# Performance work log

Hardware: AMD Instinct MI355X
Metric: run time of the kernel (lower is better)

Reference implementation:

```python
import jax, jax.numpy as jnp
import numpy as np

NTASKS = 10
CAP = 3          # semantic_cap_size / num_capsules
SEQ = 128        # max_seq_length / class_dim
HID = 768
ADAPT = 2048
NEG = -10000.0
NUM_ITERS = 3


def squash(t, axis=-1):
    sq = jnp.sum(t * t, axis=axis, keepdims=True)
    return (sq / (1.0 + sq)) * t / jnp.sqrt(sq)


def setup_inputs() -> dict:
    key = jax.random.key(0)
    ks = jax.random.split(key, 12)
    B = 128
    sc = 0.02
    return {
        "x": jax.random.normal(ks[0], (B, SEQ, HID), jnp.float32),
        "t": 5,
        "s": jnp.ones((1,), jnp.float32),
        "fc1_w": jax.random.normal(ks[1], (ADAPT, HID), jnp.float32) * sc,
        "fc1_b": jnp.zeros((ADAPT,), jnp.float32),
        "fc2_w": jax.random.normal(ks[2], (HID, ADAPT), jnp.float32) * sc,
        "fc2_b": jnp.zeros((HID,), jnp.float32),
        "efc1": jax.random.normal(ks[3], (NTASKS, ADAPT), jnp.float32),
        "efc2": jax.random.normal(ks[4], (NTASKS, HID), jnp.float32),
        "sfc1_w": jax.random.normal(ks[5], (NTASKS, 100, HID), jnp.float32) * sc,
        "sfc1_b": jnp.zeros((NTASKS, 100), jnp.float32),
        "sfc2_w": jax.random.normal(ks[6], (NTASKS, CAP, 100), jnp.float32) * sc,
        "sfc2_b": jnp.zeros((NTASKS, CAP), jnp.float32),
        "route_weights": jax.random.normal(ks[7], (CAP, NTASKS, SEQ * CAP, SEQ), jnp.float32),
        "larger_w": jax.random.normal(ks[8], (HID, CAP), jnp.float32) * sc,
        "larger_b": jnp.zeros((HID,), jnp.float32),
        "elarger": jax.random.normal(ks[9], (NTASKS, HID), jnp.float32),
    }


def reference(x, t, s, fc1_w, fc1_b, fc2_w, fc2_b, efc1, efc2,
              sfc1_w, sfc1_b, sfc2_w, sfc2_b, route_weights,
              larger_w, larger_b, elarger):
    B = x.shape[0]
    # ---- semantic capsules: per-task two-layer linear (no activation) ----
    h1 = jnp.einsum('blh,nkh->nblk', x, sfc1_w) + sfc1_b[:, None, None, :]     # [N,B,L,100]
    sem = jnp.einsum('nblk,nck->nblc', h1, sfc2_w) + sfc2_b[:, None, None, :]  # [N,B,L,C]
    # torch: cat of per-task views [B, L*C, 1] along last dim -> [B, L*C, N]
    sem = jnp.transpose(sem, (1, 2, 3, 0)).reshape(B, SEQ * CAP, NTASKS)
    sem = squash(sem, axis=-1)                 # squash over task axis
    sem = jnp.transpose(sem, (0, 2, 1))        # [B, N, L*C]

    # ---- tsv capsules: dynamic routing-by-agreement ----
    # priors[c,b,n,0,l] = sum_d sem[b,n,d] * route_weights[c,n,d,l]
    priors = jnp.einsum('bnd,cndl->cbnl', sem, route_weights)[:, :, :, None, :]  # [C,B,N,1,L]
    tsv = jnp.tril(jnp.ones((NTASKS, NTASKS), x.dtype))
    tsv_row = tsv[t].reshape(1, 1, NTASKS, 1, 1)                                  # [1,1,N,1,1]
    route_mask = jnp.where(tsv_row == 0, jnp.asarray(NEG, x.dtype), 0.0)

    logits = jnp.zeros_like(priors)
    vote_outputs = None
    for i in range(NUM_ITERS):
        logits = logits * tsv_row + route_mask
        probs = jax.nn.softmax(logits, axis=2)
        vote_outputs = jnp.sum(probs * priors, axis=2, keepdims=True)  # [C,B,1,1,L]
        outputs = squash(vote_outputs, axis=-1)
        if i != NUM_ITERS - 1:
            logits = logits + jnp.sum(priors * outputs, axis=-1, keepdims=True)

    # torch .view(B, L, -1) on contiguous [C,B,1,1,L] (row-major reshape)
    h_out = vote_outputs.reshape(B, SEQ, CAP)
    h_out = h_out @ larger_w.T + larger_b                       # [B,L,HID]
    glarger = jax.nn.sigmoid(s * elarger[t])                    # [HID]
    capsule_output = h_out * glarger

    # ---- masked adapter over (x + capsule_output) ----
    h = x + capsule_output
    gfc1 = jax.nn.sigmoid(s * efc1[t])
    gfc2 = jax.nn.sigmoid(s * efc2[t])
    h = jax.nn.relu(h @ fc1_w.T + fc1_b) * gfc1
    h = jax.nn.relu(h @ fc2_w.T + fc2_b) * gfc2
    return x + h
```

## Files before the change

kernel.cpp:

```cpp
#include <hip/hip_runtime.h>
#include <hip/hip_bf16.h>
#include <math.h>
#include <stdint.h>

typedef __bf16 bf16;
typedef __bf16 bf16x8 __attribute__((ext_vector_type(8)));
typedef __bf16 bf16x4 __attribute__((ext_vector_type(4)));
typedef float  f32x4  __attribute__((ext_vector_type(4)));

#define NTASKS 10
#define CAP    3
#define SEQ    128
#define HID    768
#define ADAPT  2048
#define BATCH  128
#define BL     (BATCH*SEQ)
#define NEGV   (-10000.0f)

__device__ __forceinline__ float sigmoidf_(float z) { return 1.f / (1.f + expf(-z)); }

__device__ __forceinline__ void gld16(const void* g, void* l) {
    auto gp = (const __attribute__((address_space(1))) uint32_t*)g;
    auto lp = (__attribute__((address_space(3))) uint32_t*)(uint32_t)(uintptr_t)l;
    __builtin_amdgcn_global_load_lds(gp, lp, 16, 0, 0);
}

__global__ void k_gates(const float* efc1, const float* efc2, const float* elarger,
                        const float* s, const int* tptr,
                        float* gfc1, float* gfc2, float* glarger) {
    int i = blockIdx.x * 256 + threadIdx.x;
    int t = *tptr; float sv = *s;
    if (i < ADAPT)                gfc1[i] = sigmoidf_(sv * efc1[t * ADAPT + i]);
    else if (i < ADAPT + HID)     { int j = i - ADAPT;        gfc2[j]    = sigmoidf_(sv * efc2[t * HID + j]); }
    else if (i < ADAPT + 2 * HID) { int j = i - ADAPT - HID;  glarger[j] = sigmoidf_(sv * elarger[t * HID + j]); }
}

__global__ void k_fusew(const float* sfc1_w, const float* sfc1_b,
                        const float* sfc2_w, const float* sfc2_b,
                        bf16* Wb, float* bb) {
    int j = blockIdx.x;
    int n = j / CAP;
    if (j >= 30) {
        for (int i = threadIdx.x; i < HID; i += 256) Wb[j * HID + i] = (bf16)0.f;
        if (threadIdx.x == 0) bb[j] = 0.f;
        return;
    }
    __shared__ float w2[100];
    if (threadIdx.x < 100) w2[threadIdx.x] = sfc2_w[j * 100 + threadIdx.x];
    __syncthreads();
    const float* w1 = sfc1_w + (size_t)n * 100 * HID;
    float a0 = 0, a1 = 0, a2 = 0;
    for (int k = 0; k < 100; ++k) {
        float s2 = w2[k];
        const float* r = w1 + k * HID;
        a0 += s2 * r[threadIdx.x];
        a1 += s2 * r[threadIdx.x + 256];
        a2 += s2 * r[threadIdx.x + 512];
    }
    Wb[j * HID + threadIdx.x]       = (bf16)a0;
    Wb[j * HID + threadIdx.x + 256] = (bf16)a1;
    Wb[j * HID + threadIdx.x + 512] = (bf16)a2;
    if (threadIdx.x == 0) {
        float b = sfc2_b[j];
        for (int k = 0; k < 100; ++k) b += sfc1_b[n * 100 + k] * w2[k];
        bb[j] = b;
    }
}

__global__ void k_convert(const float* fc1_w, const float* fc2_w, bf16* B1, bf16* B2) {
    int i = blockIdx.x * 256 + threadIdx.x;
    const int quarter = ADAPT * HID / 4;
    if (i < quarter) {
        float4 v = ((const float4*)fc1_w)[i];
        bf16x4 o = { (bf16)v.x, (bf16)v.y, (bf16)v.z, (bf16)v.w };
        ((bf16x4*)B1)[i] = o;
    } else if (i < 2 * quarter) {
        int j = i - quarter;
        float4 v = ((const float4*)fc2_w)[j];
        bf16x4 o = { (bf16)v.x, (bf16)v.y, (bf16)v.z, (bf16)v.w };
        ((bf16x4*)B2)[j] = o;
    }
}

__global__ void k_rwT(const float* __restrict__ rw, bf16* __restrict__ rwb) {
    int cn = blockIdx.x;
    int d0 = blockIdx.y * 64;
    __shared__ float t[64][129];
    const float* src = rw + (size_t)cn * 384 * 128;
    int tid = threadIdx.x;
    #pragma unroll
    for (int p = 0; p < 8; ++p) {
        int f4 = tid + p * 256;
        int row = f4 >> 5, c4 = (f4 & 31) * 4;
        float4 v = *(const float4*)(src + (size_t)(d0 + row) * 128 + c4);
        t[row][c4] = v.x; t[row][c4 + 1] = v.y; t[row][c4 + 2] = v.z; t[row][c4 + 3] = v.w;
    }
    __syncthreads();
    bf16* dst = rwb + (size_t)cn * 128 * 384 + d0;
    #pragma unroll
    for (int p = 0; p < 4; ++p) {
        int i8 = tid + p * 256;
        int l = i8 >> 3, d8 = (i8 & 7) * 8;
        bf16x8 o;
        #pragma unroll
        for (int i = 0; i < 8; ++i) o[i] = (bf16)t[d8 + i][l];
        *(bf16x8*)(dst + (size_t)l * 384 + d8) = o;
    }
}

__launch_bounds__(256)
__global__ void k_semg(const float* __restrict__ x, const bf16* __restrict__ Wb,
                       const float* __restrict__ bb, bf16* __restrict__ semb) {
    __shared__ __align__(16) bf16 As[64 * 32];
    __shared__ __align__(16) bf16 Bs[32 * 32];
    __shared__ float sem_s[64][33];
    const int tid = threadIdx.x;
    const int wave = tid >> 6, lane = tid & 63;
    const int tm = blockIdx.x;
    const int lr = lane & 15, kg = (lane >> 4) * 8;
    f32x4 acc[2] = {};

    const float* xbase = x + (size_t)(tm * 64 + (tid >> 2)) * HID + (tid & 3) * 8;
    const bf16* wbase = Wb + (size_t)(tid >> 2) * HID + (tid & 3) * 8;
    bf16* BsW = Bs + wave * 512;

    for (int k0 = 0; k0 < HID; k0 += 32) {
        float xv[8];
        *(float4*)&xv[0] = *(const float4*)(xbase + k0);
        *(float4*)&xv[4] = *(const float4*)(xbase + k0 + 4);
        __syncthreads();
        if (tid < 128) gld16(wbase + k0, BsW);
        bf16x8 xb;
        #pragma unroll
        for (int i = 0; i < 8; ++i) xb[i] = (bf16)xv[i];
        *(bf16x8*)&As[tid * 8] = xb;
        __syncthreads();
        bf16x8 af = *(const bf16x8*)&As[(wave * 16 + lr) * 32 + kg];
        bf16x8 b0 = *(const bf16x8*)&Bs[lr * 32 + kg];
        bf16x8 b1 = *(const bf16x8*)&Bs[(16 + lr) * 32 + kg];
        acc[0] = __builtin_amdgcn_mfma_f32_16x16x32_bf16(af, b0, acc[0], 0, 0, 0);
        acc[1] = __builtin_amdgcn_mfma_f32_16x16x32_bf16(af, b1, acc[1], 0, 0, 0);
    }

    #pragma unroll
    for (int n = 0; n < 2; ++n) {
        int col = n * 16 + lr;
        float bv = bb[col];
        #pragma unroll
        for (int r = 0; r < 4; ++r) {
            int row = wave * 16 + (lane >> 4) * 4 + r;
            sem_s[row][col] = acc[n][r] + bv;
        }
    }
    __syncthreads();
    if (tid < 64) {
        int bl = tm * 64 + tid;
        int b = bl >> 7, l = bl & 127;
        float vals[30];
        float sq[3] = {0.f, 0.f, 0.f};
        #pragma unroll
        for (int j = 0; j < 30; ++j) { float v = sem_s[tid][j]; vals[j] = v; sq[j % 3] += v * v; }
        float scl[3];
        #pragma unroll
        for (int c = 0; c < 3; ++c) scl[c] = (sq[c] / (1.f + sq[c])) / sqrtf(sq[c]);
        #pragma unroll
        for (int j = 0; j < 30; ++j)
            semb[((size_t)(j / 3) * BATCH + b) * 384 + l * 3 + (j % 3)] = (bf16)(vals[j] * scl[j % 3]);
    }
}

__launch_bounds__(256)
__global__ void k_priorsG(const bf16* __restrict__ semb, const bf16* __restrict__ rwb,
                          float* __restrict__ priors) {
    __shared__ __align__(16) bf16 As[128 * 32];
    __shared__ __align__(16) bf16 Bs[128 * 32];
    const int cn = blockIdx.x;
    const int c = cn / NTASKS, n = cn % NTASKS;
    const int tid = threadIdx.x;
    const int wave = tid >> 6, lane = tid & 63;
    const int wr = wave >> 1, wc = wave & 1;
    const int lr = lane & 15, kg = (lane >> 4) * 8;
    const int K = 384;
    f32x4 acc[4][4] = {};

    const bf16* Abase = semb + ((size_t)n * BATCH + (tid >> 2)) * K + (tid & 3) * 8;
    const bf16* Bbase = rwb + ((size_t)cn * 128 + (tid >> 2)) * K + (tid & 3) * 8;
    bf16* AsW = As + wave * 512;
    bf16* BsW = Bs + wave * 512;

    for (int k0 = 0; k0 < K; k0 += 32) {
        __syncthreads();
        gld16(Abase + k0, AsW);
        gld16(Abase + k0 + (size_t)64 * K, AsW + 2048);
        gld16(Bbase + k0, BsW);
        gld16(Bbase + k0 + (size_t)64 * K, BsW + 2048);
        __syncthreads();
        bf16x8 af[4], bfr[4];
        #pragma unroll
        for (int m = 0; m < 4; ++m)
            af[m] = *(const bf16x8*)&As[(wr * 64 + m * 16 + lr) * 32 + kg];
        #pragma unroll
        for (int nn = 0; nn < 4; ++nn)
            bfr[nn] = *(const bf16x8*)&Bs[(wc * 64 + nn * 16 + lr) * 32 + kg];
        #pragma unroll
        for (int m = 0; m < 4; ++m)
            #pragma unroll
            for (int nn = 0; nn < 4; ++nn)
                acc[m][nn] = __builtin_amdgcn_mfma_f32_16x16x32_bf16(af[m], bfr[nn], acc[m][nn], 0, 0, 0);
    }

    #pragma unroll
    for (int nn = 0; nn < 4; ++nn) {
        int col = wc * 64 + nn * 16 + lr;
        #pragma unroll
        for (int m = 0; m < 4; ++m) {
            int row0 = wr * 64 + m * 16 + (lane >> 4) * 4;
            #pragma unroll
            for (int r = 0; r < 4; ++r) {
                int row = row0 + r;
                priors[(((size_t)c * BATCH + row) * NTASKS + n) * 128 + col] = acc[m][nn][r];
            }
        }
    }
}

__global__ void k_routing(const float* __restrict__ priors, const int* tptr,
                          float* __restrict__ vote) {
    int cb = blockIdx.x;
    int lane = threadIdx.x;
    int t = *tptr;
    float p0[NTASKS], p1[NTASKS], ln[NTASKS];
    const float* pb = priors + (size_t)cb * NTASKS * 128;
    #pragma unroll
    for (int n = 0; n < NTASKS; ++n) {
        p0[n] = pb[n * 128 + lane];
        p1[n] = pb[n * 128 + 64 + lane];
        ln[n] = 0.f;
    }
    float v0 = 0.f, v1 = 0.f;
    for (int it = 0; it < 3; ++it) {
        float lm[NTASKS];
        float mx = -3.4e38f;
        #pragma unroll
        for (int n = 0; n < NTASKS; ++n) { lm[n] = (n <= t) ? ln[n] : NEGV; mx = fmaxf(mx, lm[n]); }
        float e[NTASKS], se = 0.f;
        #pragma unroll
        for (int n = 0; n < NTASKS; ++n) { e[n] = expf(lm[n] - mx); se += e[n]; }
        float inv = 1.f / se;
        v0 = 0.f; v1 = 0.f;
        #pragma unroll
        for (int n = 0; n < NTASKS; ++n) { float pr = e[n] * inv; v0 += pr * p0[n]; v1 += pr * p1[n]; }
        if (it == 2) break;
        float sq = v0 * v0 + v1 * v1;
        #pragma unroll
        for (int m = 32; m >= 1; m >>= 1) sq += __shfl_xor(sq, m);
        float scale = (sq / (1.f + sq)) / sqrtf(sq);
        float o0 = v0 * scale, o1 = v1 * scale;
        #pragma unroll
        for (int n = 0; n < NTASKS; ++n) {
            float d = p0[n] * o0 + p1[n] * o1;
            #pragma unroll
            for (int m = 32; m >= 1; m >>= 1) d += __shfl_xor(d, m);
            ln[n] = lm[n] + d;
        }
    }
    vote[(size_t)cb * 128 + lane]      = v0;
    vote[(size_t)cb * 128 + 64 + lane] = v1;
}

__global__ void k_buildH(const float* __restrict__ x, const float* __restrict__ vote,
                         const float* __restrict__ lw, const float* __restrict__ lb,
                         const float* __restrict__ glarger, bf16* __restrict__ H) {
    int idx = blockIdx.x * 256 + threadIdx.x;
    int bl = idx / 192, h4 = (idx % 192) * 4;
    float v0 = vote[bl * 3 + 0], v1 = vote[bl * 3 + 1], v2 = vote[bl * 3 + 2];
    float xa[4];
    *(float4*)xa = ((const float4*)x)[idx];
    bf16x4 o;
    #pragma unroll
    for (int r = 0; r < 4; ++r) {
        int hid = h4 + r;
        float hv = v0 * lw[hid * 3] + v1 * lw[hid * 3 + 1] + v2 * lw[hid * 3 + 2] + lb[hid];
        o[r] = (bf16)(xa[r] + hv * glarger[hid]);
    }
    ((bf16x4*)H)[idx] = o;
}

template <int MODE>
__launch_bounds__(512, 4)
__global__ void k_gemmW(const bf16* __restrict__ A, const bf16* __restrict__ Bw,
                        const float* __restrict__ bias, const float* __restrict__ gate,
                        const float* __restrict__ X, void* __restrict__ Out,
                        int K, int N, int TN, int NT) {
    __shared__ __align__(16) char smem[73728];
    const int tid = threadIdx.x;
    const int lane = tid & 63, w = tid >> 6;
    const int lr = lane & 15, kq = lane >> 4;
    const int qr = w >> 2, qc = w & 3;
    const int nwg = gridDim.x, bid = blockIdx.x;
    const int cpx = nwg >> 3;
    const int wg = (bid & 7) * cpx + (bid >> 3);
    const int tm = wg / TN, tn = wg % TN;

    const int srow = lane >> 2;
    const int schunk = (lane & 3) ^ ((lane >> 3) & 3);
    const bf16* Ab  = A  + (size_t)(tm * 128 + w * 16 + srow) * K + schunk * 8;
    const bf16* Bb0 = Bw + (size_t)(tn * 256 + w * 16 + srow) * K + schunk * 8;
    const bf16* Bb1 = Bb0 + (size_t)128 * K;
    auto As_ = [&](int buf) { return smem + buf * 8192; };
    auto Bs_ = [&](int buf) { return smem + 24576 + buf * 16384; };
    auto stage = [&](int k0, int buf) {
        gld16(Ab  + k0, As_(buf) + w * 1024);
        gld16(Bb0 + k0, Bs_(buf) + w * 1024);
        gld16(Bb1 + k0, Bs_(buf) + 8192 + w * 1024);
    };

    const int psw = (lr >> 1) & 3;
    f32x4 acc[4][4] = {};
    bf16x8 a[4], b[4];

    stage(0, 0);
    stage(32, 1);
    asm volatile("s_waitcnt vmcnt(3)" ::: "memory");
    __builtin_amdgcn_s_barrier();

    for (int T = 0; T < NT; ++T) {
        const int buf = T % 3;
        if (T + 2 < NT) stage((T + 2) * 32, (T + 2) % 3);
        const char* ab = As_(buf);
        const char* bb = Bs_(buf);
        #pragma unroll
        for (int m = 0; m < 4; ++m)
            a[m] = *(const bf16x8*)(ab + (qr * 64 + m * 16 + lr) * 64 + ((kq ^ psw) << 4));
        #pragma unroll
        for (int n = 0; n < 4; ++n)
            b[n] = *(const bf16x8*)(bb + (qc * 64 + n * 16 + lr) * 64 + ((kq ^ psw) << 4));
        asm volatile("s_waitcnt lgkmcnt(0)" ::: "memory");
        __builtin_amdgcn_sched_barrier(0);
        __builtin_amdgcn_s_setprio(1);
        #pragma unroll
        for (int m = 0; m < 4; ++m)
            #pragma unroll
            for (int n = 0; n < 4; ++n)
                acc[m][n] = __builtin_amdgcn_mfma_f32_16x16x32_bf16(a[m], b[n], acc[m][n], 0, 0, 0);
        __builtin_amdgcn_s_setprio(0);
        if (T + 2 < NT)      asm volatile("s_waitcnt vmcnt(3)" ::: "memory");
        else if (T + 1 < NT) asm volatile("s_waitcnt vmcnt(0)" ::: "memory");
        __builtin_amdgcn_s_barrier();
    }

    #pragma unroll
    for (int n = 0; n < 4; ++n) {
        int col = tn * 256 + qc * 64 + n * 16 + lr;
        float bv = bias[col], gv = gate[col];
        #pragma unroll
        for (int m = 0; m < 4; ++m) {
            int row0 = tm * 128 + qr * 64 + m * 16 + kq * 4;
            #pragma unroll
            for (int r = 0; r < 4; ++r) {
                float v = fmaxf(acc[m][n][r] + bv, 0.f) * gv;
                int row = row0 + r;
                if (MODE == 1) {
                    ((bf16*)Out)[(size_t)row * N + col] = (bf16)v;
                } else {
                    size_t o = (size_t)row * HID + col;
                    ((float*)Out)[o] = X[o] + v;
                }
            }
        }
    }
}

extern "C" void kernel_launch(void* const* d_in, const int* in_sizes, int n_in,
                              void* d_out, int out_size, void* d_ws, size_t ws_size,
                              hipStream_t stream) {
    const float* x      = (const float*)d_in[0];
    const int*   t      = (const int*)  d_in[1];
    const float* s      = (const float*)d_in[2];
    const float* fc1_w  = (const float*)d_in[3];
    const float* fc1_b  = (const float*)d_in[4];
    const float* fc2_w  = (const float*)d_in[5];
    const float* fc2_b  = (const float*)d_in[6];
    const float* efc1   = (const float*)d_in[7];
    const float* efc2   = (const float*)d_in[8];
    const float* sfc1_w = (const float*)d_in[9];
    const float* sfc1_b = (const float*)d_in[10];
    const float* sfc2_w = (const float*)d_in[11];
    const float* sfc2_b = (const float*)d_in[12];
    const float* rw     = (const float*)d_in[13];
    const float* lw     = (const float*)d_in[14];
    const float* lb     = (const float*)d_in[15];
    const float* elarger= (const float*)d_in[16];

    char* ws = (char*)d_ws;
    size_t off = 0;
    auto alloc = [&](size_t b) { void* p = ws + off; off = (off + b + 255) & ~(size_t)255; return p; };
    float* gfc1    = (float*)alloc(ADAPT * 4);
    float* gfc2    = (float*)alloc(HID * 4);
    float* glarger = (float*)alloc(HID * 4);
    bf16*  Wb      = (bf16*) alloc(32 * HID * 2);
    float* bb      = (float*)alloc(32 * 4);
    bf16*  B1      = (bf16*) alloc((size_t)ADAPT * HID * 2);
    bf16*  B2      = (bf16*) alloc((size_t)ADAPT * HID * 2);
    bf16*  semb    = (bf16*) alloc((size_t)NTASKS * BATCH * 384 * 2);
    bf16*  rwb     = (bf16*) alloc((size_t)30 * 128 * 384 * 2);
    float* priors  = (float*)alloc((size_t)CAP * BATCH * NTASKS * 128 * 4);
    float* vote    = (float*)alloc((size_t)CAP * BATCH * 128 * 4);
    bf16*  H1      = (bf16*) alloc((size_t)BL * ADAPT * 2);
    bf16*  H       = (bf16*)d_out;

    k_gates  <<<14, 256, 0, stream>>>(efc1, efc2, elarger, s, t, gfc1, gfc2, glarger);
    k_fusew  <<<32, 256, 0, stream>>>(sfc1_w, sfc1_b, sfc2_w, sfc2_b, Wb, bb);
    k_convert<<<3072, 256, 0, stream>>>(fc1_w, fc2_w, B1, B2);
    k_rwT    <<<dim3(30, 6), 256, 0, stream>>>(rw, rwb);
    k_semg   <<<BL / 64, 256, 0, stream>>>(x, Wb, bb, semb);
    k_priorsG<<<30, 256, 0, stream>>>(semb, rwb, priors);
    k_routing<<<CAP * BATCH, 64, 0, stream>>>(priors, t, vote);
    k_buildH <<<BL * 192 / 256, 256, 0, stream>>>(x, vote, lw, lb, glarger, H);
    k_gemmW<1><<<1024, 512, 0, stream>>>(H,  B1, fc1_b, gfc1, nullptr, H1,   HID,   ADAPT, 8, HID / 32);
    k_gemmW<2><<<384, 512, 0, stream>>>(H1, B2, fc2_b, gfc2, x,       d_out, ADAPT, HID,  3, ADAPT / 32);
}
```

Before: 201.5 us.

## Double-buffer LDS fragment reads to overlap with MFMA in adapter GEMMs

```diff
diff --git a/kernel.cpp b/kernel.cpp
--- a/kernel.cpp
+++ b/kernel.cpp
@@ -288,7 +288,7 @@
 
 template <int MODE>
 __launch_bounds__(512, 4)
-__global__ void k_gemmW(const bf16* __restrict__ A, const bf16* __restrict__ Bw,
+__global__ void k_gemmQ(const bf16* __restrict__ A, const bf16* __restrict__ Bw,
                         const float* __restrict__ bias, const float* __restrict__ gate,
                         const float* __restrict__ X, void* __restrict__ Out,
                         int K, int N, int TN, int NT) {
@@ -307,47 +307,68 @@
     const bf16* Ab  = A  + (size_t)(tm * 128 + w * 16 + srow) * K + schunk * 8;
     const bf16* Bb0 = Bw + (size_t)(tn * 256 + w * 16 + srow) * K + schunk * 8;
     const bf16* Bb1 = Bb0 + (size_t)128 * K;
-    auto As_ = [&](int buf) { return smem + buf * 8192; };
-    auto Bs_ = [&](int buf) { return smem + 24576 + buf * 16384; };
-    auto stage = [&](int k0, int buf) {
-        gld16(Ab  + k0, As_(buf) + w * 1024);
-        gld16(Bb0 + k0, Bs_(buf) + w * 1024);
-        gld16(Bb1 + k0, Bs_(buf) + 8192 + w * 1024);
+    auto stage = [&](int k0, int off) {
+        gld16(Ab  + k0, smem + off + w * 1024);
+        gld16(Bb0 + k0, smem + off + 8192 + w * 1024);
+        gld16(Bb1 + k0, smem + off + 16384 + w * 1024);
     };
 
-    const int psw = (lr >> 1) & 3;
+    const int rsl = (kq ^ ((lr >> 1) & 3)) << 4;
     f32x4 acc[4][4] = {};
-    bf16x8 a[4], b[4];
+    bf16x8 aA[4], bA[4], aB[4], bB[4];
+
+#define RD8(OFF, ASET, BSET)                                                       \
+    {                                                                              \
+        const char* ab_ = smem + (OFF);                                            \
+        const char* bb_ = smem + (OFF) + 8192;                                     \
+        _Pragma("unroll")                                                          \
+        for (int m = 0; m < 4; ++m)                                                \
+            ASET[m] = *(const bf16x8*)(ab_ + (qr * 64 + m * 16 + lr) * 64 + rsl);  \
+        _Pragma("unroll")                                                          \
+        for (int n = 0; n < 4; ++n)                                                \
+            BSET[n] = *(const bf16x8*)(bb_ + (qc * 64 + n * 16 + lr) * 64 + rsl);  \
+    }
 
     stage(0, 0);
-    stage(32, 1);
+    stage(32, 24576);
     asm volatile("s_waitcnt vmcnt(3)" ::: "memory");
     __builtin_amdgcn_s_barrier();
-
-    for (int T = 0; T < NT; ++T) {
-        const int buf = T % 3;
-        if (T + 2 < NT) stage((T + 2) * 32, (T + 2) % 3);
-        const char* ab = As_(buf);
-        const char* bb = Bs_(buf);
-        #pragma unroll
-        for (int m = 0; m < 4; ++m)
-            a[m] = *(const bf16x8*)(ab + (qr * 64 + m * 16 + lr) * 64 + ((kq ^ psw) << 4));
-        #pragma unroll
-        for (int n = 0; n < 4; ++n)
-            b[n] = *(const bf16x8*)(bb + (qc * 64 + n * 16 + lr) * 64 + ((kq ^ psw) << 4));
-        asm volatile("s_waitcnt lgkmcnt(0)" ::: "memory");
-        __builtin_amdgcn_sched_barrier(0);
-        __builtin_amdgcn_s_setprio(1);
-        #pragma unroll
-        for (int m = 0; m < 4; ++m)
-            #pragma unroll
-            for (int n = 0; n < 4; ++n)
-                acc[m][n] = __builtin_amdgcn_mfma_f32_16x16x32_bf16(a[m], b[n], acc[m][n], 0, 0, 0);
-        __builtin_amdgcn_s_setprio(0);
-        if (T + 2 < NT)      asm volatile("s_waitcnt vmcnt(3)" ::: "memory");
-        else if (T + 1 < NT) asm volatile("s_waitcnt vmcnt(0)" ::: "memory");
-        __builtin_amdgcn_s_barrier();
-    }
+    RD8(0, aA, bA);
+
+    int offS = 49152;
+    int offR = 24576;
+
+#define STEP(T, CA, CB, NA, NB)                                                    \
+    {                                                                              \
+        const int t_ = (T);                                                        \
+        if (t_ + 2 < NT) {                                                         \
+            stage((t_ + 2) * 32, offS);                                            \
+            asm volatile("s_waitcnt vmcnt(3)" ::: "memory");                       \
+        } else {                                                                   \
+            asm volatile("s_waitcnt vmcnt(0)" ::: "memory");                       \
+        }                                                                          \
+        asm volatile("s_waitcnt lgkmcnt(0)" ::: "memory");                         \
+        __builtin_amdgcn_s_barrier();                                              \
+        if (t_ + 1 < NT) RD8(offR, NA, NB);                                        \
+        __builtin_amdgcn_sched_barrier(0);                                         \
+        __builtin_amdgcn_s_setprio(1);                                             \
+        _Pragma("unroll")                                                          \
+        for (int m = 0; m < 4; ++m)                                                \
+            _Pragma("unroll")                                                      \
+            for (int n = 0; n < 4; ++n)                                            \
+                acc[m][n] = __builtin_amdgcn_mfma_f32_16x16x32_bf16(               \
+                    CA[m], CB[n], acc[m][n], 0, 0, 0);                             \
+        __builtin_amdgcn_s_setprio(0);                                             \
+        offS += 24576; if (offS >= 73728) offS = 0;                                \
+        offR += 24576; if (offR >= 73728) offR = 0;                                \
+    }
+
+    for (int T = 0; T < NT; T += 2) {
+        STEP(T,     aA, bA, aB, bB);
+        STEP(T + 1, aB, bB, aA, bA);
+    }
+#undef STEP
+#undef RD8
 
     #pragma unroll
     for (int n = 0; n < 4; ++n) {
@@ -417,6 +438,6 @@
     k_priorsG<<<30, 256, 0, stream>>>(semb, rwb, priors);
     k_routing<<<CAP * BATCH, 64, 0, stream>>>(priors, t, vote);
     k_buildH <<<BL * 192 / 256, 256, 0, stream>>>(x, vote, lw, lb, glarger, H);
-    k_gemmW<1><<<1024, 512, 0, stream>>>(H,  B1, fc1_b, gfc1, nullptr, H1,   HID,   ADAPT, 8, HID / 32);
-    k_gemmW<2><<<384, 512, 0, stream>>>(H1, B2, fc2_b, gfc2, x,       d_out, ADAPT, HID,  3, ADAPT / 32);
-}
+    k_gemmQ<1><<<1024, 512, 0, stream>>>(H,  B1, fc1_b, gfc1, nullptr, H1,   HID,   ADAPT, 8, HID / 32);
+    k_gemmQ<2><<<384, 512, 0, stream>>>(H1, B2, fc2_b, gfc2, x,       d_out, ADAPT, HID,  3, ADAPT / 32);
+}
```

After: 451.7 us. 2.24x slower.
